# Performance work log

Hardware: AMD Instinct MI355X
Metric: run time of the kernel (lower is better)

The kernel has to match this reference:

```python
import jax, jax.numpy as jnp
import numpy as np

VOCAB, EMB, SEQ_TOK, NHID, NLAYERS, NTOKEN = 400000, 300, 25, 256, 2, 2


def _lstm_layer(x, h0, c0, W_ih, W_hh, b_ih, b_hh):
    # x: [T, B, in], PyTorch gate order i, f, g, o
    def step(carry, xt):
        h, c = carry
        gates = xt @ W_ih.T + h @ W_hh.T + (b_ih + b_hh)
        i, f, g, o = jnp.split(gates, 4, axis=-1)
        c = jax.nn.sigmoid(f) * c + jax.nn.sigmoid(i) * jnp.tanh(g)
        h = jax.nn.sigmoid(o) * jnp.tanh(c)
        return (h, c), h
    (hT, cT), ys = jax.lax.scan(step, (h0, c0), x)
    return ys, hT, cT


def setup_inputs() -> dict:
    key = jax.random.key(0)
    ks = jax.random.split(key, 16)
    s = 0.05
    inp = {
        "input": jax.random.randint(ks[0], (1024, SEQ_TOK), 0, VOCAB),
        "h0": jnp.zeros((NLAYERS, 1024, NHID), jnp.float32),
        "c0": jnp.zeros((NLAYERS, 1024, NHID), jnp.float32),
        "emb_table": jax.random.normal(ks[1], (VOCAB, EMB), jnp.float32) * s,
        "fc_w": jax.random.normal(ks[2], (10, NHID), jnp.float32) * s,
        "fc_b": jnp.zeros((10,), jnp.float32),
        "dec_w": jax.random.normal(ks[3], (NTOKEN, 10), jnp.float32) * s,
        "dec_b": jnp.zeros((NTOKEN,), jnp.float32),
    }
    in_dims = [SEQ_TOK, NHID]
    for l in range(NLAYERS):
        inp[f"W_ih{l}"] = jax.random.normal(ks[4 + 4 * l], (4 * NHID, in_dims[l]), jnp.float32) * s
        inp[f"W_hh{l}"] = jax.random.normal(ks[5 + 4 * l], (4 * NHID, NHID), jnp.float32) * s
        inp[f"b_ih{l}"] = jnp.zeros((4 * NHID,), jnp.float32)
        inp[f"b_hh{l}"] = jnp.zeros((4 * NHID,), jnp.float32)
    return inp


def reference(input, h0, c0, emb_table, fc_w, fc_b, dec_w, dec_b,
              W_ih0, W_hh0, b_ih0, b_hh0, W_ih1, W_hh1, b_ih1, b_hh1):
    tokens = input.T                      # [25, B]
    B = tokens.shape[1]
    emb = emb_table[tokens]               # vectorized gather: [25, B, 300]
    emb = emb.reshape(300, B, 25)         # faithful to torch .view(300, B, 25)
    x = emb
    Ws = [(W_ih0, W_hh0, b_ih0, b_hh0), (W_ih1, W_hh1, b_ih1, b_hh1)]
    hs, cs = [], []
    for l in range(NLAYERS):
        x, hT, cT = _lstm_layer(x, h0[l], c0[l], *Ws[l])
        hs.append(hT); cs.append(cT)
    output = x                            # [300, B, nhid]
    hidden = (jnp.stack(hs), jnp.stack(cs))
    fc_out = jax.nn.relu(output @ fc_w.T + fc_b)  # [300, B, 10]
    decoded = fc_out[-1] @ dec_w.T + dec_b        # [B, ntoken]
    return (decoded.T, hidden[0], hidden[1])      # decoded.t(), (h, c)
```

## Files before the change

kernel.cpp:

```cpp
#include <hip/hip_runtime.h>
#include <stdint.h>

#define TSTEPS 300
#define BATCH  1024
#define MB     16
#define NWG    (BATCH / MB)
#define FRAGS_L0 36
#define FRAGS_L1 64
#define FRAGS_PW (FRAGS_L0 + FRAGS_L1)

typedef __bf16 bf16x8 __attribute__((ext_vector_type(8)));
typedef float  f32x4  __attribute__((ext_vector_type(4)));

__device__ __forceinline__ uint16_t f2bf(float f) {
  uint32_t u = __builtin_bit_cast(uint32_t, f);
  u += 0x7fffu + ((u >> 16) & 1u);
  return (uint16_t)(u >> 16);
}
__device__ __forceinline__ float bf2f(uint16_t h) {
  uint32_t u = ((uint32_t)h) << 16;
  return __builtin_bit_cast(float, u);
}
__device__ __forceinline__ float sigm(float x) { return 1.0f / (1.0f + __expf(-x)); }
__device__ __forceinline__ float tanh_(float x) {
  float e = __expf(2.0f * x);
  return (e - 1.0f) / (e + 1.0f);
}

__global__ void gather_x(const int* __restrict__ tok, const float* __restrict__ emb,
                         uint16_t* __restrict__ Xf) {
  int idx = blockIdx.x * 256 + threadIdx.x;
  int t    = idx >> 15;
  int rem  = idx & 32767;
  int wg   = rem >> 9;
  int e512 = rem & 511;
  int lane = e512 >> 3;
  int jj   = e512 & 7;
  int m = lane & 15, quad = lane >> 4;
  int k = quad * 8 + jj;
  float v = 0.0f;
  if (k < 25) {
    int b = wg * 16 + m;
    int n = (t * 1024 + b) * 25 + k;
    int s  = n / 307200;
    int r2 = n - s * 307200;
    int bb = r2 / 300;
    int e  = r2 - bb * 300;
    int token = tok[bb * 25 + s];
    v = emb[(size_t)token * 300 + e];
  }
  Xf[idx] = f2bf(v);
}

__global__ void pack_w(const float* __restrict__ Wih0, const float* __restrict__ Whh0,
                       const float* __restrict__ Wih1, const float* __restrict__ Whh1,
                       uint16_t* __restrict__ Wp) {
  int idx = blockIdx.x * 256 + threadIdx.x;
  int w   = idx / 51200;
  int rem = idx - w * 51200;
  int frag = rem >> 9;
  int e    = rem & 511;
  int lane = e >> 3, jj = e & 7;
  int nl = lane & 15, quad = lane >> 4;
  int kk = quad * 8 + jj;
  float v;
  if (frag < FRAGS_L0) {
    int ks = frag >> 2, nt = frag & 3;
    int n = nt * 256 + w * 16 + nl;
    if (ks == 0) v = (kk < 25) ? Wih0[n * 25 + kk] : 0.0f;
    else         v = Whh0[n * 256 + (ks - 1) * 32 + kk];
  } else {
    int f1 = frag - FRAGS_L0;
    int ks = f1 >> 2, nt = f1 & 3;
    int n = nt * 256 + w * 16 + nl;
    int k = ks * 32 + kk;
    v = (k < 256) ? Wih1[n * 256 + k] : Whh1[n * 256 + (k - 256)];
  }
  Wp[idx] = f2bf(v);
}

__global__ __launch_bounds__(1024, 4) void lstm_main(
    const float* __restrict__ h0in, const float* __restrict__ c0in,
    const float* __restrict__ fcw,  const float* __restrict__ fcb,
    const float* __restrict__ decw, const float* __restrict__ decb,
    const float* __restrict__ bih0, const float* __restrict__ bhh0,
    const float* __restrict__ bih1, const float* __restrict__ bhh1,
    const uint16_t* __restrict__ Xf, const uint16_t* __restrict__ Wp,
    float* __restrict__ out) {
  __shared__ uint16_t h0s[2][16][264];
  __shared__ uint16_t h1s[2][16][264];
  __shared__ float fcs[16][10];

  const int wg   = blockIdx.x;
  const int tid  = threadIdx.x;
  const int w    = tid >> 6;
  const int lane = tid & 63;
  const int jl   = lane & 15;
  const int quad = lane >> 4;
  const int jcol = w * 16 + jl;

  for (int idx = tid; idx < 16 * 256; idx += 1024) {
    int r = idx >> 8, k = idx & 255;
    int b = wg * 16 + r;
    h0s[0][r][k] = f2bf(h0in[(size_t)b * 256 + k]);
    h1s[0][r][k] = f2bf(h0in[262144 + (size_t)b * 256 + k]);
  }
  float c0r[4], c1r[4], h0v[4], h1v[4];
#pragma unroll
  for (int r = 0; r < 4; r++) {
    size_t b = wg * 16 + quad * 4 + r;
    c0r[r] = c0in[b * 256 + jcol];
    c1r[r] = c0in[262144 + b * 256 + jcol];
  }
  float bias0[4], bias1[4];
#pragma unroll
  for (int nt = 0; nt < 4; nt++) {
    int n = nt * 256 + jcol;
    bias0[nt] = bih0[n] + bhh0[n];
    bias1[nt] = bih1[n] + bhh1[n];
  }
  __syncthreads();

  const uint4* pw = (const uint4*)Wp + (size_t)(w * FRAGS_PW) * 64 + lane;
  const uint4* px = (const uint4*)Xf;

  int p = 0;
  for (int t = 0; t < TSTEPS; t++) {
    f32x4 acc[4];
#pragma unroll
    for (int nt = 0; nt < 4; nt++)
      acc[nt] = (f32x4){bias0[nt], bias0[nt], bias0[nt], bias0[nt]};
    {
      bf16x8 afrag = __builtin_bit_cast(bf16x8, px[((size_t)t * 64 + wg) * 64 + lane]);
      bf16x8 bfrag[4];
#pragma unroll
      for (int nt = 0; nt < 4; nt++)
        bfrag[nt] = __builtin_bit_cast(bf16x8, pw[nt * 64]);
#pragma unroll
      for (int ks = 0; ks <= 8; ks++) {
        bf16x8 anext = afrag;
        bf16x8 bnext[4] = {bfrag[0], bfrag[1], bfrag[2], bfrag[3]};
        if (ks < 8) {
          anext = __builtin_bit_cast(bf16x8,
                    *(const uint4*)&h0s[p][jl][ks * 32 + quad * 8]);
#pragma unroll
          for (int nt = 0; nt < 4; nt++)
            bnext[nt] = __builtin_bit_cast(bf16x8, pw[((ks + 1) * 4 + nt) * 64]);
        }
#pragma unroll
        for (int nt = 0; nt < 4; nt++)
          acc[nt] = __builtin_amdgcn_mfma_f32_16x16x32_bf16(afrag, bfrag[nt], acc[nt], 0, 0, 0);
        afrag = anext;
#pragma unroll
        for (int nt = 0; nt < 4; nt++) bfrag[nt] = bnext[nt];
      }
    }
#pragma unroll
    for (int r = 0; r < 4; r++) {
      float gi = sigm(acc[0][r]);
      float gf = sigm(acc[1][r]);
      float gg = tanh_(acc[2][r]);
      float go = sigm(acc[3][r]);
      float c = gf * c0r[r] + gi * gg;
      c0r[r] = c;
      float h = go * tanh_(c);
      h0v[r] = h;
      h0s[1 - p][quad * 4 + r][jcol] = f2bf(h);
    }
    __syncthreads();

#pragma unroll
    for (int nt = 0; nt < 4; nt++)
      acc[nt] = (f32x4){bias1[nt], bias1[nt], bias1[nt], bias1[nt]};
    {
      bf16x8 afrag = __builtin_bit_cast(bf16x8,
                       *(const uint4*)&h0s[1 - p][jl][quad * 8]);
      bf16x8 bfrag[4];
#pragma unroll
      for (int nt = 0; nt < 4; nt++)
        bfrag[nt] = __builtin_bit_cast(bf16x8, pw[(FRAGS_L0 + nt) * 64]);
#pragma unroll
      for (int ks = 0; ks < 16; ks++) {
        bf16x8 anext = afrag;
        bf16x8 bnext[4] = {bfrag[0], bfrag[1], bfrag[2], bfrag[3]};
        if (ks < 15) {
          int ksn = ks + 1;
          const uint16_t* abase = (ksn < 8)
              ? &h0s[1 - p][jl][ksn * 32 + quad * 8]
              : &h1s[p][jl][(ksn - 8) * 32 + quad * 8];
          anext = __builtin_bit_cast(bf16x8, *(const uint4*)abase);
#pragma unroll
          for (int nt = 0; nt < 4; nt++)
            bnext[nt] = __builtin_bit_cast(bf16x8, pw[(FRAGS_L0 + ksn * 4 + nt) * 64]);
        }
#pragma unroll
        for (int nt = 0; nt < 4; nt++)
          acc[nt] = __builtin_amdgcn_mfma_f32_16x16x32_bf16(afrag, bfrag[nt], acc[nt], 0, 0, 0);
        afrag = anext;
#pragma unroll
        for (int nt = 0; nt < 4; nt++) bfrag[nt] = bnext[nt];
      }
    }
#pragma unroll
    for (int r = 0; r < 4; r++) {
      float gi = sigm(acc[0][r]);
      float gf = sigm(acc[1][r]);
      float gg = tanh_(acc[2][r]);
      float go = sigm(acc[3][r]);
      float c = gf * c1r[r] + gi * gg;
      c1r[r] = c;
      float h = go * tanh_(c);
      h1v[r] = h;
      h1s[1 - p][quad * 4 + r][jcol] = f2bf(h);
    }
    __syncthreads();
    p ^= 1;
  }

  float* outH = out + 2048;
  float* outC = out + 2048 + 524288;
#pragma unroll
  for (int r = 0; r < 4; r++) {
    size_t b = wg * 16 + quad * 4 + r;
    outH[b * 256 + jcol]          = h0v[r];
    outH[262144 + b * 256 + jcol] = h1v[r];
    outC[b * 256 + jcol]          = c0r[r];
    outC[262144 + b * 256 + jcol] = c1r[r];
  }
  if (tid < 160) {
    int r = tid / 10, ju = tid - r * 10;
    float s = fcb[ju];
    for (int k = 0; k < 256; k++)
      s += bf2f(h1s[p][r][k]) * fcw[ju * 256 + k];
    fcs[r][ju] = fmaxf(s, 0.0f);
  }
  __syncthreads();
  if (tid < 32) {
    int r = tid & 15, m = tid >> 4;
    float d = decb[m];
#pragma unroll
    for (int q = 0; q < 10; q++) d += fcs[r][q] * decw[m * 10 + q];
    out[(size_t)m * 1024 + wg * 16 + r] = d;
  }
}

extern "C" void kernel_launch(void* const* d_in, const int* in_sizes, int n_in,
                              void* d_out, int out_size, void* d_ws, size_t ws_size,
                              hipStream_t stream) {
  const int*   tok  = (const int*)d_in[0];
  const float* h0   = (const float*)d_in[1];
  const float* c0   = (const float*)d_in[2];
  const float* emb  = (const float*)d_in[3];
  const float* fcw  = (const float*)d_in[4];
  const float* fcb  = (const float*)d_in[5];
  const float* decw = (const float*)d_in[6];
  const float* decb = (const float*)d_in[7];
  const float* Wih0 = (const float*)d_in[8];
  const float* Whh0 = (const float*)d_in[9];
  const float* bih0 = (const float*)d_in[10];
  const float* bhh0 = (const float*)d_in[11];
  const float* Wih1 = (const float*)d_in[12];
  const float* Whh1 = (const float*)d_in[13];
  const float* bih1 = (const float*)d_in[14];
  const float* bhh1 = (const float*)d_in[15];

  uint16_t* Xf  = (uint16_t*)d_ws;
  uint16_t* Wpk = Xf + 9830400;

  gather_x<<<38400, 256, 0, stream>>>(tok, emb, Xf);
  pack_w<<<3200, 256, 0, stream>>>(Wih0, Whh0, Wih1, Whh1, Wpk);
  lstm_main<<<NWG, 1024, 0, stream>>>(h0, c0, fcw, fcb, decw, decb,
                                      bih0, bhh0, bih1, bhh1, Xf, Wpk,
                                      (float*)d_out);
}
```

Before: 13.35 ms.

## Prefetch weight fragments three k-steps ahead with rotating register ring across timesteps

```diff
diff --git a/kernel.cpp b/kernel.cpp
--- a/kernel.cpp
+++ b/kernel.cpp
@@ -124,97 +124,107 @@
   const uint4* pw = (const uint4*)Wp + (size_t)(w * FRAGS_PW) * 64 + lane;
   const uint4* px = (const uint4*)Xf;
 
+  bf16x8 bq[3][4];
+#pragma unroll
+  for (int s = 0; s < 3; s++)
+#pragma unroll
+    for (int nt = 0; nt < 4; nt++)
+      bq[s][nt] = __builtin_bit_cast(bf16x8, pw[(s * 4 + nt) * 64]);
+  bf16x8 xfrag = __builtin_bit_cast(bf16x8, px[(size_t)(0 * 64 + wg) * 64 + lane]);
+  bf16x8 xnext;
+
   int p = 0;
-  for (int t = 0; t < TSTEPS; t++) {
-    f32x4 acc[4];
-#pragma unroll
-    for (int nt = 0; nt < 4; nt++)
-      acc[nt] = (f32x4){bias0[nt], bias0[nt], bias0[nt], bias0[nt]};
-    {
-      bf16x8 afrag = __builtin_bit_cast(bf16x8, px[((size_t)t * 64 + wg) * 64 + lane]);
-      bf16x8 bfrag[4];
+  for (int tm = 0; tm < TSTEPS / 3; tm++) {
+#pragma unroll
+    for (int sub = 0; sub < 3; sub++) {
+      const int t  = tm * 3 + sub;
+      const int gb = sub * 25;
+
+      f32x4 acc[4];
 #pragma unroll
       for (int nt = 0; nt < 4; nt++)
-        bfrag[nt] = __builtin_bit_cast(bf16x8, pw[nt * 64]);
-#pragma unroll
-      for (int ks = 0; ks <= 8; ks++) {
+        acc[nt] = (f32x4){bias0[nt], bias0[nt], bias0[nt], bias0[nt]};
+
+      bf16x8 afrag = xfrag;
+#pragma unroll
+      for (int ks = 0; ks < 9; ks++) {
+        const int slot = (gb + ks) % 3;
         bf16x8 anext = afrag;
-        bf16x8 bnext[4] = {bfrag[0], bfrag[1], bfrag[2], bfrag[3]};
-        if (ks < 8) {
+        if (ks < 8)
           anext = __builtin_bit_cast(bf16x8,
                     *(const uint4*)&h0s[p][jl][ks * 32 + quad * 8]);
 #pragma unroll
+        for (int nt = 0; nt < 4; nt++)
+          acc[nt] = __builtin_amdgcn_mfma_f32_16x16x32_bf16(afrag, bq[slot][nt], acc[nt], 0, 0, 0);
+        {
+          const int fo = ((gb + ks + 3) % 25) * 4;
+#pragma unroll
           for (int nt = 0; nt < 4; nt++)
-            bnext[nt] = __builtin_bit_cast(bf16x8, pw[((ks + 1) * 4 + nt) * 64]);
-        }
-#pragma unroll
-        for (int nt = 0; nt < 4; nt++)
-          acc[nt] = __builtin_amdgcn_mfma_f32_16x16x32_bf16(afrag, bfrag[nt], acc[nt], 0, 0, 0);
+            bq[slot][nt] = __builtin_bit_cast(bf16x8, pw[(fo + nt) * 64]);
+        }
         afrag = anext;
-#pragma unroll
-        for (int nt = 0; nt < 4; nt++) bfrag[nt] = bnext[nt];
-      }
-    }
-#pragma unroll
-    for (int r = 0; r < 4; r++) {
-      float gi = sigm(acc[0][r]);
-      float gf = sigm(acc[1][r]);
-      float gg = tanh_(acc[2][r]);
-      float go = sigm(acc[3][r]);
-      float c = gf * c0r[r] + gi * gg;
-      c0r[r] = c;
-      float h = go * tanh_(c);
-      h0v[r] = h;
-      h0s[1 - p][quad * 4 + r][jcol] = f2bf(h);
-    }
-    __syncthreads();
-
-#pragma unroll
-    for (int nt = 0; nt < 4; nt++)
-      acc[nt] = (f32x4){bias1[nt], bias1[nt], bias1[nt], bias1[nt]};
-    {
-      bf16x8 afrag = __builtin_bit_cast(bf16x8,
-                       *(const uint4*)&h0s[1 - p][jl][quad * 8]);
-      bf16x8 bfrag[4];
+      }
+#pragma unroll
+      for (int r = 0; r < 4; r++) {
+        float gi = sigm(acc[0][r]);
+        float gf = sigm(acc[1][r]);
+        float gg = tanh_(acc[2][r]);
+        float go = sigm(acc[3][r]);
+        float c = gf * c0r[r] + gi * gg;
+        c0r[r] = c;
+        float h = go * tanh_(c);
+        h0v[r] = h;
+        h0s[1 - p][quad * 4 + r][jcol] = f2bf(h);
+      }
+      __syncthreads();
+
 #pragma unroll
       for (int nt = 0; nt < 4; nt++)
-        bfrag[nt] = __builtin_bit_cast(bf16x8, pw[(FRAGS_L0 + nt) * 64]);
+        acc[nt] = (f32x4){bias1[nt], bias1[nt], bias1[nt], bias1[nt]};
+
+      afrag = __builtin_bit_cast(bf16x8, *(const uint4*)&h0s[1 - p][jl][quad * 8]);
 #pragma unroll
       for (int ks = 0; ks < 16; ks++) {
+        const int slot = (gb + 9 + ks) % 3;
+        if (ks == 0) {
+          int tn = (t + 1 < TSTEPS) ? t + 1 : 0;
+          xnext = __builtin_bit_cast(bf16x8, px[(size_t)(tn * 64 + wg) * 64 + lane]);
+        }
         bf16x8 anext = afrag;
-        bf16x8 bnext[4] = {bfrag[0], bfrag[1], bfrag[2], bfrag[3]};
         if (ks < 15) {
-          int ksn = ks + 1;
+          const int ksn = ks + 1;
           const uint16_t* abase = (ksn < 8)
               ? &h0s[1 - p][jl][ksn * 32 + quad * 8]
               : &h1s[p][jl][(ksn - 8) * 32 + quad * 8];
           anext = __builtin_bit_cast(bf16x8, *(const uint4*)abase);
+        }
+#pragma unroll
+        for (int nt = 0; nt < 4; nt++)
+          acc[nt] = __builtin_amdgcn_mfma_f32_16x16x32_bf16(afrag, bq[slot][nt], acc[nt], 0, 0, 0);
+        {
+          const int fo = ((gb + 9 + ks + 3) % 25) * 4;
 #pragma unroll
           for (int nt = 0; nt < 4; nt++)
-            bnext[nt] = __builtin_bit_cast(bf16x8, pw[(FRAGS_L0 + ksn * 4 + nt) * 64]);
-        }
-#pragma unroll
-        for (int nt = 0; nt < 4; nt++)
-          acc[nt] = __builtin_amdgcn_mfma_f32_16x16x32_bf16(afrag, bfrag[nt], acc[nt], 0, 0, 0);
+            bq[slot][nt] = __builtin_bit_cast(bf16x8, pw[(fo + nt) * 64]);
+        }
         afrag = anext;
-#pragma unroll
-        for (int nt = 0; nt < 4; nt++) bfrag[nt] = bnext[nt];
-      }
+      }
+#pragma unroll
+      for (int r = 0; r < 4; r++) {
+        float gi = sigm(acc[0][r]);
+        float gf = sigm(acc[1][r]);
+        float gg = tanh_(acc[2][r]);
+        float go = sigm(acc[3][r]);
+        float c = gf * c1r[r] + gi * gg;
+        c1r[r] = c;
+        float h = go * tanh_(c);
+        h1v[r] = h;
+        h1s[1 - p][quad * 4 + r][jcol] = f2bf(h);
+      }
+      __syncthreads();
+      p ^= 1;
+      xfrag = xnext;
     }
-#pragma unroll
-    for (int r = 0; r < 4; r++) {
-      float gi = sigm(acc[0][r]);
-      float gf = sigm(acc[1][r]);
-      float gg = tanh_(acc[2][r]);
-      float go = sigm(acc[3][r]);
-      float c = gf * c1r[r] + gi * gg;
-      c1r[r] = c;
-      float h = go * tanh_(c);
-      h1v[r] = h;
-      h1s[1 - p][quad * 4 + r][jcol] = f2bf(h);
-    }
-    __syncthreads();
-    p ^= 1;
   }
 
   float* outH = out + 2048;
```

Result: slower. 14.06 ms (+5.3%).
